# Performance work log

Measured on AMD Instinct MI355X. Metric: run time of the kernel, lower is better.

## Reference

```python
import jax, jax.numpy as jnp
import numpy as np

B, T, D, H, TW = 4, 4096, 2560, 10, 4
C_CONST = 8.0  # RG-LRU 'c' constant from the paper/code


def setup_inputs() -> dict:
    key = jax.random.key(0)
    ks = jax.random.split(key, 8)
    s = 1.0 / np.sqrt(D)  # variance_scaling fan_in
    Dh = D // H
    return dict(
        x=jax.random.normal(ks[0], (B, T, D), jnp.float32),
        segment_pos=jnp.tile(jnp.arange(T, dtype=jnp.int32), (B, 1)),
        Wy=(jax.random.normal(ks[1], (D, D), jnp.float32) * s),
        by=jnp.zeros((D,), jnp.float32),
        Wx=(jax.random.normal(ks[2], (D, D), jnp.float32) * s),
        bx=jnp.zeros((D,), jnp.float32),
        conv_w=(jax.random.normal(ks[3], (TW, D), jnp.float32) * (1.0 / np.sqrt(TW))),
        conv_b=jnp.zeros((D,), jnp.float32),
        a_param=jax.random.uniform(ks[4], (D,), jnp.float32, minval=-4.0, maxval=-3.0),
        ig_w=(jax.random.normal(ks[5], (H, Dh, Dh), jnp.float32) * (1.0 / np.sqrt(Dh))),
        ig_b=jnp.zeros((H, Dh), jnp.float32),
        ag_w=(jax.random.normal(ks[6], (H, Dh, Dh), jnp.float32) * (1.0 / np.sqrt(Dh))),
        ag_b=jnp.zeros((H, Dh), jnp.float32),
        Wo=(jax.random.normal(ks[7], (D, D), jnp.float32) * s),
        bo=jnp.zeros((D,), jnp.float32),
    )


def _block_diag_linear(x, w, b):
    # x: [B,T,D]; w: [H,Dh,Dh]; b: [H,Dh]
    Bb, Tt, Dd = x.shape
    Hh = w.shape[0]
    xh = x.reshape(Bb, Tt, Hh, -1)
    yh = jnp.einsum('bthd,hdk->bthk', xh, w) + b
    return yh.reshape(Bb, Tt, Dd)


def _forward(x, segment_pos, Wy, by, Wx, bx, conv_w, conv_b, a_param,
             ig_w, ig_b, ag_w, ag_b, Wo, bo):
    # Gate branch: dense + gelu
    y = jax.nn.gelu(x @ Wy + by)
    # Main branch: dense
    xb = x @ Wx + bx
    # Causal depthwise conv1d (left zero pad), w[TW-1] multiplies current token
    tw = conv_w.shape[0]
    seq = xb.shape[1]
    xp = jnp.pad(xb, ((0, 0), (tw - 1, 0), (0, 0)))
    conv = conv_b[None, None]
    for i in range(tw):
        conv = conv + conv_w[i][None, None] * xp[:, i:i + seq]
    # RG-LRU
    reset = (segment_pos == 0)[..., None]  # [B,T,1]
    gate_x = jax.nn.sigmoid(_block_diag_linear(conv, ig_w, ig_b))
    gate_a = jax.nn.sigmoid(_block_diag_linear(conv, ag_w, ag_b))
    log_a = -C_CONST * gate_a * jax.nn.softplus(a_param)  # [B,T,D]
    a = jnp.exp(log_a)
    multiplier = jnp.sqrt(1.0 - jnp.exp(2.0 * log_a))
    multiplier = jnp.where(reset, 1.0, multiplier)
    norm_x = conv * gate_x * multiplier
    a = jnp.where(reset, 0.0, a)
    # diagonal linear scan: h_t = a_t * h_{t-1} + norm_x_t
    def step(h, inp):
        a_t, x_t = inp
        h = a_t * h + x_t
        return h, h
    h0 = jnp.zeros((x.shape[0], a.shape[-1]), a.dtype)
    _, hs = jax.lax.scan(step, h0, (jnp.swapaxes(a, 0, 1), jnp.swapaxes(norm_x, 0, 1)))
    h = jnp.swapaxes(hs, 0, 1)  # [B,T,D]
    # elementwise gate and output projection
    return (h * y) @ Wo + bo


def reference(x, segment_pos, Wy, by, Wx, bx, conv_w, conv_b, a_param,
              ig_w, ig_b, ag_w, ag_b, Wo, bo):
    return _forward(x, segment_pos, Wy, by, Wx, bx, conv_w, conv_b, a_param,
                    ig_w, ig_b, ag_w, ag_b, Wo, bo)
```

## Files before the change

kernel.cpp:

```cpp
#include <hip/hip_runtime.h>

#define D_DIM 2560
#define T_DIM 4096
#define B_DIM 4
#define H_DIM 10
#define DH 256
#define TW_DIM 4
#define M_DIM (B_DIM * T_DIM)
#define CHUNKS 64
#define TC (T_DIM / CHUNKS)

typedef _Float16 f16;
typedef __attribute__((ext_vector_type(8))) _Float16 f16x8;
typedef __attribute__((ext_vector_type(4))) _Float16 f16x4;
typedef __attribute__((ext_vector_type(2))) _Float16 f16x2;
typedef __attribute__((ext_vector_type(4))) float f32x4;
typedef __attribute__((ext_vector_type(2))) float f32x2;

__global__ void cvt_f16_kernel(const float* __restrict__ in, f16* __restrict__ out, long n4) {
  long i = (long)blockIdx.x * blockDim.x + threadIdx.x;
  if (i >= n4) return;
  f32x4 v = ((const f32x4*)in)[i];
  f16x4 o;
  o[0] = (f16)v[0]; o[1] = (f16)v[1]; o[2] = (f16)v[2]; o[3] = (f16)v[3];
  ((f16x4*)out)[i] = o;
}

__global__ void transpose_cvt3_kernel(const float* __restrict__ s0, const float* __restrict__ s1,
                                      const float* __restrict__ s2, f16* __restrict__ out,
                                      int R, int C) {
  __shared__ float tile[32][33];
  const int z = blockIdx.z;
  const float* in = (z == 0) ? s0 : ((z == 1) ? s1 : s2);
  out += (long)z * R * C;
  int c0 = blockIdx.x * 32, r0 = blockIdx.y * 32;
  int tx = threadIdx.x, ty = threadIdx.y;
  for (int i = ty; i < 32; i += 8)
    tile[i][tx] = in[(long)(r0 + i) * C + (c0 + tx)];
  __syncthreads();
  for (int i = ty; i < 32; i += 8)
    out[(long)(c0 + i) * R + (r0 + tx)] = (f16)tile[tx][i];
}

__global__ void transpose_cvt2_kernel(const float* __restrict__ sa, const float* __restrict__ sb,
                                      f16* __restrict__ out, int R, int C, int half) {
  __shared__ float tile[32][33];
  const int z = blockIdx.z;
  const float* in = (z < half) ? (sa + (long)z * R * C) : (sb + (long)(z - half) * R * C);
  out += (long)z * R * C;
  int c0 = blockIdx.x * 32, r0 = blockIdx.y * 32;
  int tx = threadIdx.x, ty = threadIdx.y;
  for (int i = ty; i < 32; i += 8)
    tile[i][tx] = in[(long)(r0 + i) * C + (c0 + tx)];
  __syncthreads();
  for (int i = ty; i < 32; i += 8)
    out[(long)(c0 + i) * R + (r0 + tx)] = (f16)tile[tx][i];
}

__device__ __forceinline__ void async_cp16(const void* g, void* l) {
  __builtin_amdgcn_global_load_lds(
      (const __attribute__((address_space(1))) unsigned int*)g,
      (__attribute__((address_space(3))) unsigned int*)l, 16, 0, 0);
}

__device__ __forceinline__ float fast_sigmoid(float v) {
  return 1.f / (1.f + __expf(-v));
}

#define BM2 256
#define BN2 256
#define BK2 32

template<int ACT, int OUT16>
__global__ __launch_bounds__(512, 2)
void gemm256_kernel(const f16* __restrict__ A, long ldA,
                    const f16* __restrict__ Bt, long ldB,
                    const float* __restrict__ bias,
                    void* __restrict__ Cv, long ldC, int K) {
  __shared__ __attribute__((aligned(16))) f16 sm[4 * 16384];
  const int tid = threadIdx.x;
  const int wave = tid >> 6;
  const int lane = tid & 63;
  const int wm = wave >> 2;
  const int wn = wave & 3;

  const int nx_ = gridDim.x;
  const int nwg = nx_ * gridDim.y;
  int lid = blockIdx.y * nx_ + blockIdx.x;
  lid = (lid & 7) * (nwg >> 3) + (lid >> 3);
  const long bm = (long)(lid / nx_) * BM2;
  const long bn = (long)(lid % nx_) * BN2;

  const int sRow = wave * 16 + (lane >> 2);
  const int sChunk = (lane & 3) ^ ((lane >> 2) & 3) ^ ((lane >> 4) & 3);
  const int sOff = sChunk * 8;
  const f16* pA0 = A + (bm + sRow) * ldA + sOff;
  const f16* pA1 = pA0 + 128 * ldA;
  const f16* pB0 = Bt + (bn + sRow) * ldB + sOff;
  const f16* pB1 = pB0 + 128 * ldB;
  const int wOff = wave * 512;

  const int quad = lane >> 4, l16 = lane & 15;
  const int rswz = (quad ^ (l16 & 3) ^ ((l16 >> 2) & 3)) * 8;
  const int aRowBase = (wm * 128 + l16) * BK2 + rswz;
  const int bRowBase = (wn * 64 + l16) * BK2 + rswz;

  f32x4 acc[8][4];
#pragma unroll
  for (int i = 0; i < 8; ++i)
#pragma unroll
    for (int j = 0; j < 4; ++j) {
      acc[i][j][0] = 0.f; acc[i][j][1] = 0.f; acc[i][j][2] = 0.f; acc[i][j][3] = 0.f;
    }

  const int NT = K / BK2;

#pragma unroll
  for (int p = 0; p < 3; ++p) {
    f16* dst = sm + p * 16384;
    const int kp = (p < NT ? p : NT - 1) * BK2;
    async_cp16(pA0 + kp, dst + wOff);
    async_cp16(pA1 + kp, dst + 4096 + wOff);
    async_cp16(pB0 + kp, dst + 8192 + wOff);
    async_cp16(pB1 + kp, dst + 12288 + wOff);
  }
  asm volatile("s_waitcnt vmcnt(8)" ::: "memory");
  __builtin_amdgcn_s_barrier();

#pragma unroll 4
  for (int t = 0; t < NT; ++t) {
    const f16* As = sm + (t & 3) * 16384;
    const f16* Bs = As + 8192;
    const int kp = (t + 3 < NT ? t + 3 : NT - 1) * BK2;
    f16* dst = sm + ((t + 3) & 3) * 16384;

    f16x8 af0[4], bf[4];
#pragma unroll
    for (int i = 0; i < 4; ++i) af0[i] = *(const f16x8*)&As[aRowBase + i * 16 * BK2];
#pragma unroll
    for (int j = 0; j < 4; ++j) bf[j]  = *(const f16x8*)&Bs[bRowBase + j * 16 * BK2];
    async_cp16(pA0 + kp, dst + wOff);
    async_cp16(pA1 + kp, dst + 4096 + wOff);
    __builtin_amdgcn_s_setprio(1);
#pragma unroll
    for (int i = 0; i < 4; ++i)
#pragma unroll
      for (int j = 0; j < 4; ++j)
        acc[i][j] = __builtin_amdgcn_mfma_f32_16x16x32_f16(af0[i], bf[j], acc[i][j], 0, 0, 0);
    __builtin_amdgcn_s_setprio(0);

    f16x8 af1[4];
#pragma unroll
    for (int i = 0; i < 4; ++i) af1[i] = *(const f16x8*)&As[aRowBase + (64 + i * 16) * BK2];
    async_cp16(pB0 + kp, dst + 8192 + wOff);
    async_cp16(pB1 + kp, dst + 12288 + wOff);
    __builtin_amdgcn_s_setprio(1);
#pragma unroll
    for (int i = 0; i < 4; ++i)
#pragma unroll
      for (int j = 0; j < 4; ++j)
        acc[4 + i][j] = __builtin_amdgcn_mfma_f32_16x16x32_f16(af1[i], bf[j], acc[4 + i][j], 0, 0, 0);
    __builtin_amdgcn_s_setprio(0);

    asm volatile("s_waitcnt vmcnt(8)" ::: "memory");
    __builtin_amdgcn_s_barrier();
  }

#pragma unroll
  for (int i = 0; i < 8; ++i) {
    const long row0 = bm + wm * 128 + i * 16 + quad * 4;
#pragma unroll
    for (int j = 0; j < 4; ++j) {
      const long colIn = bn + wn * 64 + j * 16 + l16;
      const float bv = bias[colIn];
#pragma unroll
      for (int r = 0; r < 4; ++r) {
        const long row = row0 + r;
        float v = acc[i][j][r] + bv;
        if (ACT == 1) {
          const float u = v;
          const float tt = 0.7978845608028654f * (u + 0.044715f * u * u * u);
          v = u * fast_sigmoid(2.f * tt);
        }
        const long cidx = row * ldC + colIn;
        if (OUT16) ((f16*)Cv)[cidx] = (f16)v;
        else       ((float*)Cv)[cidx] = v;
      }
    }
  }
}

#define BM 128
#define BN 128
#define BK 32

__global__ __launch_bounds__(256, 2)
void gemm_gates_kernel(const f16* __restrict__ A, long ldA,
                       const f16* __restrict__ igt, const f16* __restrict__ agt,
                       const float* __restrict__ igb, const float* __restrict__ agb,
                       const float* __restrict__ apar, const int* __restrict__ segp,
                       f16* __restrict__ aOut, f16* __restrict__ nxOut, int K) {
  __shared__ __attribute__((aligned(16))) f16 As[BM * BK];
  __shared__ __attribute__((aligned(16))) f16 B1s[BN * BK];
  __shared__ __attribute__((aligned(16))) f16 B2s[BN * BK];
  const int tid = threadIdx.x;
  const int wave = tid >> 6;
  const int lane = tid & 63;
  const int wm = wave >> 1, wn = wave & 1;
  const long bm = (long)blockIdx.y * BM;
  const long bn = (long)blockIdx.x * BN;
  const int z = blockIdx.z;
  const f16* Az = A + (long)z * DH;
  const f16* B1 = igt + (long)z * DH * DH;
  const f16* B2 = agt + (long)z * DH * DH;
  const float* b1 = igb + (long)z * DH;
  const float* b2 = agb + (long)z * DH;
  const long cColOff = (long)z * DH;

  const int sRow = wave * 32 + (lane >> 2);
  const int sCol = ((lane & 3) ^ (sRow & 3) ^ ((sRow >> 2) & 3)) * 8;
  const f16* gA = Az + (bm + sRow) * ldA + sCol;
  const f16* gB1 = B1 + (bn + sRow) * (long)K + sCol;
  const f16* gB2 = B2 + (bn + sRow) * (long)K + sCol;
  f16* lA = As + wave * 1024;
  f16* lB1 = B1s + wave * 1024;
  f16* lB2 = B2s + wave * 1024;

  f32x4 accI[4][4], accA[4][4];
#pragma unroll
  for (int i = 0; i < 4; ++i)
#pragma unroll
    for (int j = 0; j < 4; ++j) {
      accI[i][j][0] = 0.f; accI[i][j][1] = 0.f; accI[i][j][2] = 0.f; accI[i][j][3] = 0.f;
      accA[i][j][0] = 0.f; accA[i][j][1] = 0.f; accA[i][j][2] = 0.f; accA[i][j][3] = 0.f;
    }

  const int quad = lane >> 4, l16 = lane & 15;
  const int rswz = (quad ^ (l16 & 3) ^ ((l16 >> 2) & 3)) * 8;

  for (int k0 = 0; k0 < K; k0 += BK) {
    async_cp16(gA, lA);
    async_cp16(gA + 16 * ldA, lA + 512);
    async_cp16(gB1, lB1);
    async_cp16(gB1 + 16 * (long)K, lB1 + 512);
    async_cp16(gB2, lB2);
    async_cp16(gB2 + 16 * (long)K, lB2 + 512);
    gA += BK; gB1 += BK; gB2 += BK;
    __syncthreads();
    f16x8 af[4], bf1[4], bf2[4];
#pragma unroll
    for (int i = 0; i < 4; ++i) {
      af[i]  = *(const f16x8*)&As[(wm * 64 + i * 16 + l16) * BK + rswz];
      bf1[i] = *(const f16x8*)&B1s[(wn * 64 + i * 16 + l16) * BK + rswz];
      bf2[i] = *(const f16x8*)&B2s[(wn * 64 + i * 16 + l16) * BK + rswz];
    }
#pragma unroll
    for (int i = 0; i < 4; ++i)
#pragma unroll
      for (int j = 0; j < 4; ++j) {
        accI[i][j] = __builtin_amdgcn_mfma_f32_16x16x32_f16(af[i], bf1[j], accI[i][j], 0, 0, 0);
        accA[i][j] = __builtin_amdgcn_mfma_f32_16x16x32_f16(af[i], bf2[j], accA[i][j], 0, 0, 0);
      }
    __syncthreads();
  }

#pragma unroll
  for (int i = 0; i < 4; ++i) {
    const long row0 = bm + wm * 64 + i * 16 + quad * 4;
#pragma unroll
    for (int j = 0; j < 4; ++j) {
      const long colIn = bn + wn * 64 + j * 16 + l16;
      const long colG = cColOff + colIn;
      const float bv1 = b1[colIn];
      const float bv2 = b2[colIn];
      const float sp = log1pf(__expf(apar[colG]));
#pragma unroll
      for (int r = 0; r < 4; ++r) {
        const long row = row0 + r;
        const float gx = fast_sigmoid(accI[i][j][r] + bv1);
        const float ga = fast_sigmoid(accA[i][j][r] + bv2);
        const float log_a = -8.f * ga * sp;
        float a = __expf(log_a);
        float mult = sqrtf(fmaxf(1.f - __expf(2.f * log_a), 0.f));
        if (segp[row] == 0) { a = 0.f; mult = 1.f; }
        const long cidx = row * D_DIM + colG;
        const float cv = (float)A[row * ldA + colG];
        aOut[cidx] = (f16)a;
        nxOut[cidx] = (f16)(cv * gx * mult);
      }
    }
  }
}

__global__ void conv_kernel(const f16* __restrict__ xb, const float* __restrict__ cw,
                            const float* __restrict__ cb, f16* __restrict__ out) {
  const int d4 = blockIdx.x * 128 + threadIdx.x;
  const int t = blockIdx.y;
  const int b = blockIdx.z;
  const long idx4 = ((long)b * T_DIM + t) * (D_DIM / 4) + d4;
  f32x4 acc = ((const f32x4*)cb)[d4];
#pragma unroll
  for (int i = 0; i < TW_DIM; ++i) {
    const int tt = t - (TW_DIM - 1) + i;
    if (tt >= 0) {
      f16x4 xv = ((const f16x4*)xb)[idx4 + (long)(i - (TW_DIM - 1)) * (D_DIM / 4)];
      f32x4 w = ((const f32x4*)cw)[i * (D_DIM / 4) + d4];
      acc[0] += w[0] * (float)xv[0];
      acc[1] += w[1] * (float)xv[1];
      acc[2] += w[2] * (float)xv[2];
      acc[3] += w[3] * (float)xv[3];
    }
  }
  f16x4 o;
  o[0] = (f16)acc[0]; o[1] = (f16)acc[1]; o[2] = (f16)acc[2]; o[3] = (f16)acc[3];
  ((f16x4*)out)[idx4] = o;
}

__global__ void scanA_kernel(const f16* __restrict__ a16, const f16* __restrict__ nx16,
                             float* __restrict__ Ac, float* __restrict__ Sc) {
  const int d2 = blockIdx.x * 256 + threadIdx.x;
  const int c = blockIdx.y;
  const int b = blockIdx.z;
  long base2 = ((long)b * T_DIM + (long)c * TC) * (D_DIM / 2) + d2;
  float Ap0 = 1.f, Ap1 = 1.f, S0 = 0.f, S1 = 0.f;
  for (int t = 0; t < TC; ++t) {
    f16x2 av = ((const f16x2*)a16)[base2];
    f16x2 xv = ((const f16x2*)nx16)[base2];
    S0 = (float)av[0] * S0 + (float)xv[0];
    S1 = (float)av[1] * S1 + (float)xv[1];
    Ap0 *= (float)av[0];
    Ap1 *= (float)av[1];
    base2 += D_DIM / 2;
  }
  const long cidx2 = ((long)b * CHUNKS + c) * (D_DIM / 2) + d2;
  f32x2 av_; av_[0] = Ap0; av_[1] = Ap1;
  f32x2 sv_; sv_[0] = S0; sv_[1] = S1;
  ((f32x2*)Ac)[cidx2] = av_;
  ((f32x2*)Sc)[cidx2] = sv_;
}

__global__ void scanB_kernel(const float* __restrict__ Ac, const float* __restrict__ Sc,
                             float* __restrict__ He) {
  const int d = blockIdx.x * 256 + threadIdx.x;
  const int b = blockIdx.z;
  float h = 0.f;
  for (int c = 0; c < CHUNKS; ++c) {
    const long cidx = ((long)b * CHUNKS + c) * D_DIM + d;
    He[cidx] = h;
    h = Ac[cidx] * h + Sc[cidx];
  }
}

__global__ void scanC_kernel(const f16* __restrict__ a16, const f16* __restrict__ nx16,
                             const float* __restrict__ He, const f16* __restrict__ y16,
                             f16* __restrict__ hy16) {
  const int d2 = blockIdx.x * 256 + threadIdx.x;
  const int c = blockIdx.y;
  const int b = blockIdx.z;
  long base2 = ((long)b * T_DIM + (long)c * TC) * (D_DIM / 2) + d2;
  f32x2 hv = ((const f32x2*)He)[((long)b * CHUNKS + c) * (D_DIM / 2) + d2];
  float h0 = hv[0], h1 = hv[1];
  for (int t = 0; t < TC; ++t) {
    f16x2 av = ((const f16x2*)a16)[base2];
    f16x2 xv = ((const f16x2*)nx16)[base2];
    f16x2 yv = ((const f16x2*)y16)[base2];
    h0 = (float)av[0] * h0 + (float)xv[0];
    h1 = (float)av[1] * h1 + (float)xv[1];
    f16x2 o;
    o[0] = (f16)(h0 * (float)yv[0]);
    o[1] = (f16)(h1 * (float)yv[1]);
    ((f16x2*)hy16)[base2] = o;
    base2 += D_DIM / 2;
  }
}

extern "C" void kernel_launch(void* const* d_in, const int* in_sizes, int n_in,
                              void* d_out, int out_size, void* d_ws, size_t ws_size,
                              hipStream_t stream) {
  const float* x   = (const float*)d_in[0];
  const int*   segp= (const int*)d_in[1];
  const float* Wy  = (const float*)d_in[2];
  const float* by  = (const float*)d_in[3];
  const float* Wx  = (const float*)d_in[4];
  const float* bx  = (const float*)d_in[5];
  const float* cw  = (const float*)d_in[6];
  const float* cb  = (const float*)d_in[7];
  const float* ap  = (const float*)d_in[8];
  const float* igw = (const float*)d_in[9];
  const float* igb = (const float*)d_in[10];
  const float* agw = (const float*)d_in[11];
  const float* agb = (const float*)d_in[12];
  const float* Wo  = (const float*)d_in[13];
  const float* bo  = (const float*)d_in[14];
  float* out = (float*)d_out;
  char* ws = (char*)d_ws;

  const long MD = (long)M_DIM * D_DIM;
  f16*   x16    = (f16*)(ws + 0);
  f16*   a16    = (f16*)(ws + 0);
  f16*   y16    = (f16*)(ws + MD * 2);
  f16*   xb2    = (f16*)(ws + MD * 4);
  f16*   hy16   = (f16*)(ws + MD * 4);
  f16*   conv16 = (f16*)(ws + MD * 6);
  f16*   nx16   = (f16*)(ws + MD * 8);
  long off = MD * 10;
  f16* Wt  = (f16*)(ws + off); off += 3L * D_DIM * D_DIM * 2;
  f16* igagt = (f16*)(ws + off); off += 20L * DH * DH * 2;
  float* Ac = (float*)(ws + off); off += (long)B_DIM * CHUNKS * D_DIM * 4;
  float* Sc = (float*)(ws + off); off += (long)B_DIM * CHUNKS * D_DIM * 4;
  float* He = (float*)(ws + off); off += (long)B_DIM * CHUNKS * D_DIM * 4;
  f16* Wyt = Wt;
  f16* Wxt = Wt + (long)D_DIM * D_DIM;
  f16* Wot = Wt + 2L * D_DIM * D_DIM;
  f16* igt = igagt;
  f16* agt = igagt + 10L * DH * DH;

  dim3 tb(32, 8);
  cvt_f16_kernel<<<dim3((unsigned)(MD / 4 / 256)), 256, 0, stream>>>(x, x16, MD / 4);
  transpose_cvt3_kernel<<<dim3(80, 80, 3), tb, 0, stream>>>(Wy, Wx, Wo, Wt, D_DIM, D_DIM);
  transpose_cvt2_kernel<<<dim3(8, 8, 20), tb, 0, stream>>>(igw, agw, igagt, DH, DH, 10);
  gemm256_kernel<1, 1><<<dim3(10, 64, 1), 512, 0, stream>>>(
      x16, D_DIM, Wyt, D_DIM, by, (void*)y16, D_DIM, D_DIM);
  gemm256_kernel<0, 1><<<dim3(10, 64, 1), 512, 0, stream>>>(
      x16, D_DIM, Wxt, D_DIM, bx, (void*)xb2, D_DIM, D_DIM);
  conv_kernel<<<dim3(5, 4096, 4), 128, 0, stream>>>(xb2, cw, cb, conv16);
  gemm_gates_kernel<<<dim3(2, 128, 10), 256, 0, stream>>>(
      conv16, D_DIM, igt, agt, igb, agb, ap, segp, a16, nx16, DH);
  scanA_kernel<<<dim3(5, CHUNKS, 4), 256, 0, stream>>>(a16, nx16, Ac, Sc);
  scanB_kernel<<<dim3(10, 1, 4), 256, 0, stream>>>(Ac, Sc, He);
  scanC_kernel<<<dim3(5, CHUNKS, 4), 256, 0, stream>>>(a16, nx16, He, y16, hy16);
  gemm256_kernel<0, 0><<<dim3(10, 64, 1), 512, 0, stream>>>(
      hy16, D_DIM, Wot, D_DIM, bo, (void*)out, D_DIM, D_DIM);
}
```

Baseline: 1.358 ms.

## Restructure 256x256 GEMM main loop into 8-phase ping-pong schedule with BK=64

Rewrites the large GEMM mainloop to use K-tiles of 64 with two LDS buffers and an explicit 8-phase schedule that interleaves LDS reads, async global-to-LDS staging of A/B halves, and MFMA quadrants separated by barriers and priority changes. A new XOR swizzle over 8 chunks replaces the old 4-chunk swizzle. The aim is to hide global load latency and LDS bank conflicts behind MFMA work with finer-grained overlap. In exchange it adds many more barriers per iteration and assumes K is a multiple of 128.

```diff
diff --git a/kernel.cpp b/kernel.cpp
--- a/kernel.cpp
+++ b/kernel.cpp
@@ -69,7 +69,6 @@
 
 #define BM2 256
 #define BN2 256
-#define BK2 32
 
 template<int ACT, int OUT16>
 __global__ __launch_bounds__(512, 2)
@@ -77,7 +76,7 @@
                     const f16* __restrict__ Bt, long ldB,
                     const float* __restrict__ bias,
                     void* __restrict__ Cv, long ldC, int K) {
-  __shared__ __attribute__((aligned(16))) f16 sm[4 * 16384];
+  __shared__ __attribute__((aligned(16))) f16 smh[65536];
   const int tid = threadIdx.x;
   const int wave = tid >> 6;
   const int lane = tid & 63;
@@ -91,20 +90,30 @@
   const long bm = (long)(lid / nx_) * BM2;
   const long bn = (long)(lid % nx_) * BN2;
 
-  const int sRow = wave * 16 + (lane >> 2);
-  const int sChunk = (lane & 3) ^ ((lane >> 2) & 3) ^ ((lane >> 4) & 3);
-  const int sOff = sChunk * 8;
-  const f16* pA0 = A + (bm + sRow) * ldA + sOff;
-  const f16* pA1 = pA0 + 128 * ldA;
-  const f16* pB0 = Bt + (bn + sRow) * ldB + sOff;
-  const f16* pB1 = pB0 + 128 * ldB;
-  const int wOff = wave * 512;
+  const int rsub = lane >> 3;
+  const int gc8 = (((lane & 7) ^ rsub) & 7) * 8;
+  const f16* gA0 = A + (bm + wave * 16 + rsub) * ldA + gc8;
+  const f16* gB0 = Bt + (bn + wave * 16 + rsub) * ldB + gc8;
+  const int wls = wave * 1024;
+
+#define STG_A(buf, al, ko) do { \
+  async_cp16(gA0 + ((al) * 128) * ldA + (ko), smh + (buf) * 32768 + (al) * 8192 + wls); \
+  async_cp16(gA0 + ((al) * 128 + 8) * ldA + (ko), smh + (buf) * 32768 + (al) * 8192 + wls + 512); \
+} while (0)
+#define STG_B(buf, bl, ko) do { \
+  async_cp16(gB0 + ((bl) * 128) * ldB + (ko), smh + (buf) * 32768 + 16384 + (bl) * 8192 + wls); \
+  async_cp16(gB0 + ((bl) * 128 + 8) * ldB + (ko), smh + (buf) * 32768 + 16384 + (bl) * 8192 + wls + 512); \
+} while (0)
 
   const int quad = lane >> 4, l16 = lane & 15;
-  const int rswz = (quad ^ (l16 & 3) ^ ((l16 >> 2) & 3)) * 8;
-  const int aRowBase = (wm * 128 + l16) * BK2 + rswz;
-  const int bRowBase = (wn * 64 + l16) * BK2 + rswz;
-
+  const int sw0 = ((quad ^ (l16 & 7)) & 7) * 8;
+  const int sw1 = (((4 + quad) ^ (l16 & 7)) & 7) * 8;
+  const int aRB0 = wm * 8192 + l16 * 64;
+  const int aRB1 = 32768 + aRB0;
+  const int bRB0 = 16384 + (wn >> 1) * 8192 + ((wn & 1) * 64 + l16) * 64;
+  const int bRB1 = 32768 + bRB0;
+
+  f16x8 aF[4][2], bF[4][2];
   f32x4 acc[8][4];
 #pragma unroll
   for (int i = 0; i < 8; ++i)
@@ -113,58 +122,57 @@
       acc[i][j][0] = 0.f; acc[i][j][1] = 0.f; acc[i][j][2] = 0.f; acc[i][j][3] = 0.f;
     }
 
-  const int NT = K / BK2;
-
-#pragma unroll
-  for (int p = 0; p < 3; ++p) {
-    f16* dst = sm + p * 16384;
-    const int kp = (p < NT ? p : NT - 1) * BK2;
-    async_cp16(pA0 + kp, dst + wOff);
-    async_cp16(pA1 + kp, dst + 4096 + wOff);
-    async_cp16(pB0 + kp, dst + 8192 + wOff);
-    async_cp16(pB1 + kp, dst + 12288 + wOff);
-  }
-  asm volatile("s_waitcnt vmcnt(8)" ::: "memory");
+#define RD_AQ(base, off) do { _Pragma("unroll") for (int m_ = 0; m_ < 4; ++m_) { \
+  aF[m_][0] = *(const f16x8*)&smh[(base) + (off) + m_ * 1024 + sw0]; \
+  aF[m_][1] = *(const f16x8*)&smh[(base) + (off) + m_ * 1024 + sw1]; } } while (0)
+#define RD_B2(base, n0) do { _Pragma("unroll") for (int n_ = 0; n_ < 2; ++n_) { \
+  bF[(n0) + n_][0] = *(const f16x8*)&smh[(base) + ((n0) + n_) * 1024 + sw0]; \
+  bF[(n0) + n_][1] = *(const f16x8*)&smh[(base) + ((n0) + n_) * 1024 + sw1]; } } while (0)
+#define MMQ(m0, n0) do { _Pragma("unroll") for (int m_ = 0; m_ < 4; ++m_) \
+  _Pragma("unroll") for (int n_ = 0; n_ < 2; ++n_) \
+    acc[(m0) + m_][(n0) + n_] = __builtin_amdgcn_mfma_f32_16x16x32_f16(aF[m_][1], bF[(n0) + n_][1], \
+      __builtin_amdgcn_mfma_f32_16x16x32_f16(aF[m_][0], bF[(n0) + n_][0], acc[(m0) + m_][(n0) + n_], 0, 0, 0), 0, 0, 0); \
+} while (0)
+#define PH_MID() \
+  __builtin_amdgcn_s_barrier(); \
+  asm volatile("s_waitcnt lgkmcnt(0)" ::: "memory"); \
+  __builtin_amdgcn_sched_barrier(0); \
+  __builtin_amdgcn_s_setprio(1)
+#define PH_END() \
+  __builtin_amdgcn_s_setprio(0); \
+  __builtin_amdgcn_s_barrier(); \
+  __builtin_amdgcn_sched_barrier(0)
+#define PH_END_VM() \
+  __builtin_amdgcn_s_setprio(0); \
+  asm volatile("s_waitcnt vmcnt(4)" ::: "memory"); \
+  __builtin_amdgcn_s_barrier(); \
+  __builtin_amdgcn_sched_barrier(0)
+
+  STG_A(1, 0, 64); STG_A(1, 1, 64);
+  STG_B(0, 0, 0);  STG_B(0, 1, 0);
+  STG_A(0, 0, 0);  STG_A(0, 1, 0);
+  STG_B(1, 0, 64); STG_B(1, 1, 64);
+  asm volatile("s_waitcnt vmcnt(4)" ::: "memory");
   __builtin_amdgcn_s_barrier();
-
-#pragma unroll 4
-  for (int t = 0; t < NT; ++t) {
-    const f16* As = sm + (t & 3) * 16384;
-    const f16* Bs = As + 8192;
-    const int kp = (t + 3 < NT ? t + 3 : NT - 1) * BK2;
-    f16* dst = sm + ((t + 3) & 3) * 16384;
-
-    f16x8 af0[4], bf[4];
-#pragma unroll
-    for (int i = 0; i < 4; ++i) af0[i] = *(const f16x8*)&As[aRowBase + i * 16 * BK2];
-#pragma unroll
-    for (int j = 0; j < 4; ++j) bf[j]  = *(const f16x8*)&Bs[bRowBase + j * 16 * BK2];
-    async_cp16(pA0 + kp, dst + wOff);
-    async_cp16(pA1 + kp, dst + 4096 + wOff);
-    __builtin_amdgcn_s_setprio(1);
-#pragma unroll
-    for (int i = 0; i < 4; ++i)
-#pragma unroll
-      for (int j = 0; j < 4; ++j)
-        acc[i][j] = __builtin_amdgcn_mfma_f32_16x16x32_f16(af0[i], bf[j], acc[i][j], 0, 0, 0);
-    __builtin_amdgcn_s_setprio(0);
-
-    f16x8 af1[4];
-#pragma unroll
-    for (int i = 0; i < 4; ++i) af1[i] = *(const f16x8*)&As[aRowBase + (64 + i * 16) * BK2];
-    async_cp16(pB0 + kp, dst + 8192 + wOff);
-    async_cp16(pB1 + kp, dst + 12288 + wOff);
-    __builtin_amdgcn_s_setprio(1);
-#pragma unroll
-    for (int i = 0; i < 4; ++i)
-#pragma unroll
-      for (int j = 0; j < 4; ++j)
-        acc[4 + i][j] = __builtin_amdgcn_mfma_f32_16x16x32_f16(af1[i], bf[j], acc[4 + i][j], 0, 0, 0);
-    __builtin_amdgcn_s_setprio(0);
-
-    asm volatile("s_waitcnt vmcnt(8)" ::: "memory");
-    __builtin_amdgcn_s_barrier();
-  }
+  __builtin_amdgcn_sched_barrier(0);
+
+  const int NIT = K / 128;
+  const int NTm1 = (K / 64) - 1;
+#pragma unroll 1
+  for (int it = 0; it < NIT; ++it) {
+    const long k1 = (long)(2 * it + 1) * 64;
+    const long k2 = (long)(2 * it + 2 <= NTm1 ? 2 * it + 2 : NTm1) * 64;
+    const long k3 = (long)(2 * it + 3 <= NTm1 ? 2 * it + 3 : NTm1) * 64;
+    RD_AQ(aRB0, 0); RD_B2(bRB0, 0); STG_A(1, 0, k1); PH_MID(); MMQ(0, 0); PH_END();
+    RD_B2(bRB0, 2); STG_A(1, 1, k1); PH_MID(); MMQ(0, 2); PH_END();
+    RD_AQ(aRB0, 4096); STG_B(0, 0, k2); PH_MID(); MMQ(4, 2); PH_END();
+    STG_B(0, 1, k2); PH_MID(); MMQ(4, 0); PH_END_VM();
+    RD_AQ(aRB1, 0); RD_B2(bRB1, 0); STG_A(0, 0, k2); PH_MID(); MMQ(0, 0); PH_END();
+    RD_B2(bRB1, 2); STG_A(0, 1, k2); PH_MID(); MMQ(0, 2); PH_END();
+    RD_AQ(aRB1, 4096); STG_B(1, 0, k3); PH_MID(); MMQ(4, 2); PH_END();
+    STG_B(1, 1, k3); PH_MID(); MMQ(4, 0); PH_END_VM();
+  }
+  asm volatile("s_waitcnt vmcnt(0)" ::: "memory");
 
 #pragma unroll
   for (int i = 0; i < 8; ++i) {
@@ -188,6 +196,14 @@
       }
     }
   }
+#undef STG_A
+#undef STG_B
+#undef RD_AQ
+#undef RD_B2
+#undef MMQ
+#undef PH_MID
+#undef PH_END
+#undef PH_END_VM
 }
 
 #define BM 128
```

Measured after the change: 1.344 ms. About the same (-1.0%).
